# Kernel tuning notes

Measured on AMD Instinct MI355X. Metric: run time of the kernel, lower is better.

## Reference

```python
import jax, jax.numpy as jnp
import numpy as np

N_REC = 3
TEMP = 1.0
BAL_W = 0.01
Z_W = 0.001


def setup_inputs() -> dict:
    key = jax.random.key(0)
    kx, kw = jax.random.split(key)
    x = jax.random.normal(kx, (4, 4096, 2048), dtype=jnp.float32)
    W = 0.02 * jax.random.normal(kw, (N_REC, 2048), dtype=jnp.float32)  # nn.Linear(d_model, n_rec, bias=False), std=0.02
    return {"x": x, "W": W, "recursion_idx": 0}


def _compact(mask, cur_gate, max_k):
    """Vectorized version of the per-batch nonzero/pad loop.
    mask: [B,T] bool, cur_gate: [B,T] float. Returns sel [B,max_k], gv [B,max_k]."""
    counts = jnp.sum(mask, axis=-1)  # [B]
    # stable argsort pushes active (key=0) positions to the front, in order
    key = jnp.where(mask, 0, 1).astype(jnp.int32)
    order = jnp.argsort(key, axis=-1, stable=True)  # [B,T]
    # position j clamps to last valid index (replicates pad-with-last behavior)
    pos = jnp.minimum(jnp.arange(max_k)[None, :], jnp.maximum(counts - 1, 0)[:, None])
    sel = jnp.take_along_axis(order, pos, axis=1)  # [B,max_k]
    empty = (counts == 0)[:, None]
    sel = jnp.where(empty, 0, sel)
    gv = jnp.take_along_axis(cur_gate, sel, axis=1)
    gv = jnp.where(empty, jnp.float32(0.0), gv)
    return sel, gv


def reference(x, W, recursion_idx):
    # router linear + softmax + argmax (one-shot token-choice assignment)
    logits = jnp.einsum('btd,nd->btn', x / TEMP, W)  # [B,T,N_REC]
    gates = jax.nn.softmax(logits, axis=-1)
    assign = jnp.argmax(gates, axis=-1)  # [B,T]
    active_mask = assign >= recursion_idx
    cur_gate = gates[:, :, min(recursion_idx, N_REC - 1)]  # [B,T]
    # max_k is data-dependent (eager, outside jit)
    max_k = max(1, int(jnp.max(jnp.sum(active_mask, axis=-1))))
    sel, gv = _compact(active_mask, cur_gate, max_k)
    selected = sel[..., None]          # [B,max_k,1] int
    gate_weights = gv[..., None]       # [B,max_k,1]
    # training-mode losses (recursion_idx == 0 path)
    fracs = jnp.mean(jax.nn.one_hot(assign, N_REC, dtype=jnp.float32), axis=(0, 1))
    aux_loss = BAL_W * jnp.sum((fracs - 1.0 / N_REC) ** 2)
    z = jax.scipy.special.logsumexp(logits, axis=-1)
    z_loss = Z_W * jnp.mean(z ** 2)
    return selected, gate_weights, logits[:, :, :1], aux_loss, z_loss
```

## Files before the change

kernel.cpp:

```cpp
#include <hip/hip_runtime.h>
#include <hip/hip_bf16.h>

#define B_    4
#define T_    4096
#define D_    2048
#define NTOK  (B_ * T_)
#define NREC  3
#define BAL_W 0.01f
#define Z_W   0.001f
#define ABLK  2048
#define ATHR  256

typedef __attribute__((ext_vector_type(4))) float float4v;

__global__ __launch_bounds__(ATHR) void tcr9_phaseA(
    const float* __restrict__ x,
    const float* __restrict__ w,
    const int* __restrict__ ridx_p,
    float* __restrict__ out_f,
    float4v* __restrict__ partials)
{
    __shared__ float s_w[NREC * D_];
    {
        const float4v* src = reinterpret_cast<const float4v*>(w);
        float4v*       dst = reinterpret_cast<float4v*>(s_w);
#pragma unroll
        for (int i = 0; i < (NREC * D_ / 4) / ATHR; ++i)
            dst[i * ATHR + threadIdx.x] =
                __builtin_nontemporal_load(src + i * ATHR + threadIdx.x);
    }
    __syncthreads();

    const int ridx = ridx_p[0];
    const int jc   = ridx < (NREC - 1) ? (ridx < 0 ? 0 : ridx) : (NREC - 1);
    const int lane = threadIdx.x & 63;
    const int wv   = threadIdx.x >> 6;
    const int wid  = (blockIdx.x * ATHR + threadIdx.x) >> 6;
    const int t0   = wid * 2;

    const float* xp0 = x + (size_t)t0 * D_;
    float4v xv0[8], xv1[8];
#pragma unroll
    for (int j = 0; j < 8; ++j) {
        xv0[j] = __builtin_nontemporal_load(
            reinterpret_cast<const float4v*>(xp0 + (j * 64 + lane) * 4));
        xv1[j] = __builtin_nontemporal_load(
            reinterpret_cast<const float4v*>(xp0 + D_ + (j * 64 + lane) * 4));
    }

    float a0 = 0.f, a1 = 0.f, a2 = 0.f;
    float b0 = 0.f, b1 = 0.f, b2 = 0.f;
#pragma unroll
    for (int j = 0; j < 8; ++j) {
        const int kb = (j * 64 + lane) * 4;
        const float4v w0 = *reinterpret_cast<const float4v*>(&s_w[kb]);
        const float4v w1 = *reinterpret_cast<const float4v*>(&s_w[D_ + kb]);
        const float4v w2 = *reinterpret_cast<const float4v*>(&s_w[2 * D_ + kb]);
#pragma unroll
        for (int e = 0; e < 4; ++e) {
            a0 = fmaf(xv0[j][e], w0[e], a0);
            a1 = fmaf(xv0[j][e], w1[e], a1);
            a2 = fmaf(xv0[j][e], w2[e], a2);
            b0 = fmaf(xv1[j][e], w0[e], b0);
            b1 = fmaf(xv1[j][e], w1[e], b1);
            b2 = fmaf(xv1[j][e], w2[e], b2);
        }
    }
#pragma unroll
    for (int off = 32; off > 0; off >>= 1) {
        a0 += __shfl_xor(a0, off);
        a1 += __shfl_xor(a1, off);
        a2 += __shfl_xor(a2, off);
        b0 += __shfl_xor(b0, off);
        b1 += __shfl_xor(b1, off);
        b2 += __shfl_xor(b2, off);
    }

    __shared__ float4v s_part[(ATHR / 64) * 2];
    if ((lane & 31) == 0) {
        const int hi = lane >> 5;
        const int t  = t0 + hi;
        const float l0 = hi ? b0 : a0;
        const float l1 = hi ? b1 : a1;
        const float l2 = hi ? b2 : a2;

        const float m  = fmaxf(l0, fmaxf(l1, l2));
        const float e0 = expf(l0 - m), e1 = expf(l1 - m), e2 = expf(l2 - m);
        const float s  = e0 + e1 + e2;
        const float z  = m + logf(s);
        int   assign = 0; float best = l0;
        if (l1 > best) { best = l1; assign = 1; }
        if (l2 > best) { best = l2; assign = 2; }
        const float g = (jc == 0 ? e0 : (jc == 1 ? e1 : e2)) / s;

        out_f[NTOK + t]     = (assign >= ridx) ? g : -g;
        out_f[2 * NTOK + t] = l0;

        float4v p;
        p[0] = z * z;
        p[1] = (assign == 0) ? 1.f : 0.f;
        p[2] = (assign == 1) ? 1.f : 0.f;
        p[3] = (assign == 2) ? 1.f : 0.f;
        s_part[wv * 2 + hi] = p;
    }
    __syncthreads();
    if (threadIdx.x == 0) {
        float4v p = s_part[0];
#pragma unroll
        for (int i = 1; i < (ATHR / 64) * 2; ++i) {
            const float4v q = s_part[i];
#pragma unroll
            for (int e = 0; e < 4; ++e) p[e] += q[e];
        }
        partials[blockIdx.x] = p;
    }
}

__global__ __launch_bounds__(1024) void tcr9_phaseB(
    const float4v* __restrict__ partials,
    float* __restrict__ out_f)
{
    __shared__ int      s_ws[16];
    __shared__ unsigned s_sel[T_];
    __shared__ float    s_g[T_];
    __shared__ float4v  s_red[16];
    const int b    = blockIdx.x;
    const int tid  = threadIdx.x;
    const int lane = tid & 63;
    const int wv   = tid >> 6;
    const int base = b * T_;

    float g[4]; int f[4]; int loc = 0;
#pragma unroll
    for (int r = 0; r < 4; ++r) {
        g[r] = out_f[NTOK + base + tid * 4 + r];
        f[r] = (g[r] > 0.f) ? 1 : 0;
        loc += f[r];
    }
    int isc = loc;
#pragma unroll
    for (int off = 1; off < 64; off <<= 1) {
        const int u = __shfl_up(isc, off);
        if (lane >= off) isc += u;
    }
    if (lane == 63) s_ws[wv] = isc;
    __syncthreads();
    int wbase = 0, cnt = 0;
#pragma unroll
    for (int i = 0; i < 16; ++i) {
        const int v = s_ws[i];
        cnt += v;
        if (i < wv) wbase += v;
    }
    int pos = wbase + isc - loc;
#pragma unroll
    for (int r = 0; r < 4; ++r) {
        if (f[r] && (unsigned)pos < (unsigned)T_) {
            s_sel[pos] = (unsigned)(tid * 4 + r);
            s_g[pos]   = g[r];
            ++pos;
        }
    }
    __syncthreads();

#pragma unroll
    for (int r = 0; r < 4; ++r) {
        const int k = tid + r * 1024;
        float selv, gv;
        if (cnt == 0) { selv = 0.f; gv = 0.f; }
        else {
            const int kk = (k < cnt) ? k : (cnt - 1);
            selv = (float)s_sel[kk];
            gv   = s_g[kk];
        }
        out_f[base + k]        = selv;
        out_f[NTOK + base + k] = gv;
    }

    float4v p;
    if (b == 0) {
        const float4v pa = partials[tid];
        const float4v pb = partials[tid + 1024];
#pragma unroll
        for (int e = 0; e < 4; ++e) p[e] = pa[e] + pb[e];
    } else { p[0] = 0.f; p[1] = 0.f; p[2] = 0.f; p[3] = 0.f; }
#pragma unroll
    for (int off = 32; off > 0; off >>= 1) {
#pragma unroll
        for (int e = 0; e < 4; ++e) p[e] += __shfl_xor(p[e], off);
    }
    if (lane == 0) s_red[wv] = p;
    __syncthreads();
    if (b == 0 && tid == 0) {
        float4v q = s_red[0];
#pragma unroll
        for (int i = 1; i < 16; ++i) {
            const float4v r2 = s_red[i];
#pragma unroll
            for (int e = 0; e < 4; ++e) q[e] += r2[e];
        }
        const float inv = 1.0f / (float)NTOK;
        float aux = 0.f;
#pragma unroll
        for (int n = 0; n < NREC; ++n) {
            const float d = q[1 + n] * inv - (1.0f / 3.0f);
            aux = fmaf(d, d, aux);
        }
        out_f[3 * NTOK + 0] = BAL_W * aux;
        out_f[3 * NTOK + 1] = Z_W * q[0] * inv;
    }
}

extern "C" void kernel_launch(void* const* d_in, const int* in_sizes, int n_in,
                              void* d_out, int out_size, void* d_ws, size_t ws_size,
                              hipStream_t stream) {
    const float* x  = (const float*)d_in[0];
    const float* w  = (const float*)d_in[1];
    const int* ridx = (const int*)d_in[2];
    float* out_f = (float*)d_out;
    float4v* partials = (float4v*)d_ws;

    tcr9_phaseA<<<dim3(ABLK), dim3(ATHR), 0, stream>>>(x, w, ridx, out_f, partials);
    tcr9_phaseB<<<dim3(B_), dim3(1024), 0, stream>>>(partials, out_f);
}
```

Baseline: 31.54 us.

## Split router epilogue into separate finish kernel with partial-lane dot outputs

The streaming GEMV kernel now stops its wave reduction early, leaving four partial sums per token per expert, and writes them to a workspace buffer. A new finish kernel sums the partials and computes softmax, argmax, gate, logit output and block partial sums with one token per thread. This takes the serial per-lane epilogue and block reduction out of the bandwidth-bound streaming kernel. In exchange it adds a third kernel launch and an extra round trip of the dots buffer through memory.

```diff
diff --git a/kernel.cpp b/kernel.cpp
--- a/kernel.cpp
+++ b/kernel.cpp
@@ -10,15 +10,14 @@
 #define Z_W   0.001f
 #define ABLK  2048
 #define ATHR  256
+#define FBLK  (NTOK / 256)
 
 typedef __attribute__((ext_vector_type(4))) float float4v;
 
-__global__ __launch_bounds__(ATHR) void tcr9_phaseA(
+__global__ __launch_bounds__(ATHR) void tcr11_stream(
     const float* __restrict__ x,
     const float* __restrict__ w,
-    const int* __restrict__ ridx_p,
-    float* __restrict__ out_f,
-    float4v* __restrict__ partials)
+    float* __restrict__ dots)
 {
     __shared__ float s_w[NREC * D_];
     {
@@ -31,10 +30,7 @@
     }
     __syncthreads();
 
-    const int ridx = ridx_p[0];
-    const int jc   = ridx < (NREC - 1) ? (ridx < 0 ? 0 : ridx) : (NREC - 1);
     const int lane = threadIdx.x & 63;
-    const int wv   = threadIdx.x >> 6;
     const int wid  = (blockIdx.x * ATHR + threadIdx.x) >> 6;
     const int t0   = wid * 2;
 
@@ -67,7 +63,7 @@
         }
     }
 #pragma unroll
-    for (int off = 32; off > 0; off >>= 1) {
+    for (int off = 4; off < 64; off <<= 1) {
         a0 += __shfl_xor(a0, off);
         a1 += __shfl_xor(a1, off);
         a2 += __shfl_xor(a2, off);
@@ -75,48 +71,70 @@
         b1 += __shfl_xor(b1, off);
         b2 += __shfl_xor(b2, off);
     }
-
-    __shared__ float4v s_part[(ATHR / 64) * 2];
-    if ((lane & 31) == 0) {
-        const int hi = lane >> 5;
-        const int t  = t0 + hi;
-        const float l0 = hi ? b0 : a0;
-        const float l1 = hi ? b1 : a1;
-        const float l2 = hi ? b2 : a2;
-
-        const float m  = fmaxf(l0, fmaxf(l1, l2));
-        const float e0 = expf(l0 - m), e1 = expf(l1 - m), e2 = expf(l2 - m);
-        const float s  = e0 + e1 + e2;
-        const float z  = m + logf(s);
-        int   assign = 0; float best = l0;
-        if (l1 > best) { best = l1; assign = 1; }
-        if (l2 > best) { best = l2; assign = 2; }
-        const float g = (jc == 0 ? e0 : (jc == 1 ? e1 : e2)) / s;
-
-        out_f[NTOK + t]     = (assign >= ridx) ? g : -g;
-        out_f[2 * NTOK + t] = l0;
-
-        float4v p;
-        p[0] = z * z;
-        p[1] = (assign == 0) ? 1.f : 0.f;
-        p[2] = (assign == 1) ? 1.f : 0.f;
-        p[3] = (assign == 2) ? 1.f : 0.f;
-        s_part[wv * 2 + hi] = p;
-    }
+    if (lane < 4) {
+        float* d0 = dots + (size_t)t0 * 12 + lane * 3;
+        d0[0] = a0; d0[1] = a1; d0[2] = a2;
+        float* d1 = dots + (size_t)(t0 + 1) * 12 + lane * 3;
+        d1[0] = b0; d1[1] = b1; d1[2] = b2;
+    }
+}
+
+__global__ __launch_bounds__(256) void tcr11_finish(
+    const float* __restrict__ dots,
+    const int* __restrict__ ridx_p,
+    float* __restrict__ out_f,
+    float4v* __restrict__ partials)
+{
+    const int ridx = ridx_p[0];
+    const int jc   = ridx < (NREC - 1) ? (ridx < 0 ? 0 : ridx) : (NREC - 1);
+    const int t    = blockIdx.x * 256 + threadIdx.x;
+    const int lane = threadIdx.x & 63;
+    const int wv   = threadIdx.x >> 6;
+
+    const float4v* dp = reinterpret_cast<const float4v*>(dots + (size_t)t * 12);
+    const float4v f0 = dp[0], f1 = dp[1], f2 = dp[2];
+    const float a0 = (f0[0] + f0[3]) + (f1[2] + f2[1]);
+    const float a1 = (f0[1] + f1[0]) + (f1[3] + f2[2]);
+    const float a2 = (f0[2] + f1[1]) + (f2[0] + f2[3]);
+
+    const float m  = fmaxf(a0, fmaxf(a1, a2));
+    const float e0 = expf(a0 - m), e1 = expf(a1 - m), e2 = expf(a2 - m);
+    const float s  = e0 + e1 + e2;
+    const float z  = m + logf(s);
+    int   assign = 0; float best = a0;
+    if (a1 > best) { best = a1; assign = 1; }
+    if (a2 > best) { best = a2; assign = 2; }
+    const float g = (jc == 0 ? e0 : (jc == 1 ? e1 : e2)) / s;
+
+    out_f[NTOK + t]     = (assign >= ridx) ? g : -g;
+    out_f[2 * NTOK + t] = a0;
+
+    float4v p;
+    p[0] = z * z;
+    p[1] = (assign == 0) ? 1.f : 0.f;
+    p[2] = (assign == 1) ? 1.f : 0.f;
+    p[3] = (assign == 2) ? 1.f : 0.f;
+#pragma unroll
+    for (int off = 32; off > 0; off >>= 1) {
+#pragma unroll
+        for (int e = 0; e < 4; ++e) p[e] += __shfl_xor(p[e], off);
+    }
+    __shared__ float4v s_part[4];
+    if (lane == 0) s_part[wv] = p;
     __syncthreads();
     if (threadIdx.x == 0) {
-        float4v p = s_part[0];
-#pragma unroll
-        for (int i = 1; i < (ATHR / 64) * 2; ++i) {
-            const float4v q = s_part[i];
-#pragma unroll
-            for (int e = 0; e < 4; ++e) p[e] += q[e];
-        }
-        partials[blockIdx.x] = p;
-    }
-}
-
-__global__ __launch_bounds__(1024) void tcr9_phaseB(
+        float4v q = s_part[0];
+#pragma unroll
+        for (int i = 1; i < 4; ++i) {
+            const float4v r2 = s_part[i];
+#pragma unroll
+            for (int e = 0; e < 4; ++e) q[e] += r2[e];
+        }
+        partials[blockIdx.x] = q;
+    }
+}
+
+__global__ __launch_bounds__(1024) void tcr11_phaseB(
     const float4v* __restrict__ partials,
     float* __restrict__ out_f)
 {
@@ -178,12 +196,8 @@
     }
 
     float4v p;
-    if (b == 0) {
-        const float4v pa = partials[tid];
-        const float4v pb = partials[tid + 1024];
-#pragma unroll
-        for (int e = 0; e < 4; ++e) p[e] = pa[e] + pb[e];
-    } else { p[0] = 0.f; p[1] = 0.f; p[2] = 0.f; p[3] = 0.f; }
+    if (b == 0 && tid < FBLK) p = partials[tid];
+    else { p[0] = 0.f; p[1] = 0.f; p[2] = 0.f; p[3] = 0.f; }
 #pragma unroll
     for (int off = 32; off > 0; off >>= 1) {
 #pragma unroll
@@ -218,8 +232,11 @@
     const float* w  = (const float*)d_in[1];
     const int* ridx = (const int*)d_in[2];
     float* out_f = (float*)d_out;
+
     float4v* partials = (float4v*)d_ws;
-
-    tcr9_phaseA<<<dim3(ABLK), dim3(ATHR), 0, stream>>>(x, w, ridx, out_f, partials);
-    tcr9_phaseB<<<dim3(B_), dim3(1024), 0, stream>>>(partials, out_f);
-}
+    float*   dots     = (float*)d_ws + 1024;
+
+    tcr11_stream<<<dim3(ABLK), dim3(ATHR), 0, stream>>>(x, w, dots);
+    tcr11_finish<<<dim3(FBLK), dim3(256),  0, stream>>>(dots, ridx, out_f, partials);
+    tcr11_phaseB<<<dim3(B_),   dim3(1024), 0, stream>>>(partials, out_f);
+}
```

Measured after the change: 33.06 us. 4.8% more time.
